# Performance work log

Measured on AMD Instinct MI355X. Metric: run time of the kernel, lower is better.

The kernel has to match this reference:

```python
import jax, jax.numpy as jnp
import numpy as np

N = 32768      # nodes
DIN = 256      # in_channels (space dim; hyperbolic input has DIN+1 dims)
DOUT = 256     # out_channels
H = 8          # num_heads
K = 1.0        # Lorentz curvature manifold.k
P = 2          # power_k
EPS = 1e-6


def _lorentz(key, n, d):
    # random point on Lorentz manifold: time = sqrt(||space||^2 + k)
    s = jax.random.normal(key, (n, d), jnp.float32)
    t = jnp.sqrt(jnp.sum(s * s, -1, keepdims=True) + K)
    return jnp.concatenate([t, s], -1)


def setup_inputs() -> dict:
    key = jax.random.key(0)
    ks = jax.random.split(key, 8)
    sc = 0.02
    return {
        "query_input": _lorentz(ks[0], N, DIN),
        "source_input": _lorentz(ks[1], N, DIN),
        "Wq_w": jax.random.normal(ks[2], (H, DOUT, DIN + 1), jnp.float32) * sc,
        "Wq_b": jnp.zeros((H, DOUT), jnp.float32),
        "Wk_w": jax.random.normal(ks[3], (H, DOUT, DIN + 1), jnp.float32) * sc,
        "Wk_b": jnp.zeros((H, DOUT), jnp.float32),
        "Wv_w": jax.random.normal(ks[4], (H, DOUT, DIN + 1), jnp.float32) * sc,
        "Wv_b": jnp.zeros((H, DOUT), jnp.float32),
        "norm_scale": jnp.ones((), jnp.float32),
        "v_map_w": jax.random.normal(ks[5], (DOUT, DIN), jnp.float32) * sc,
        "v_map_b": jnp.zeros((DOUT,), jnp.float32),
        "final_w": jax.random.normal(ks[6], (DOUT, H * DOUT), jnp.float32) * sc,
        "final_b": jnp.zeros((DOUT,), jnp.float32),
    }


def _hyp_linear(x, W, b):
    # HypLinear for all heads at once. x: [N, Din+1], W: [H, Dout, Din+1], b: [H, Dout]
    xs = jnp.einsum('ni,hoi->nho', x, W) + b              # space part [N,H,Dout]
    xt = jnp.sqrt(jnp.sum(xs * xs, -1, keepdims=True) + K)  # Lorentz time
    return jnp.concatenate([xt, xs], -1)                  # [N,H,Dout+1]


def _fp(x, p=P):
    # fp(x) = ||x|| / ||x^p|| * x^p  (per-vector rescaled power map)
    norm_x = jnp.linalg.norm(x, axis=-1, keepdims=True)
    xp = x ** p
    norm_xp = jnp.linalg.norm(xp, axis=-1, keepdims=True)
    return norm_x / norm_xp * xp


def reference(query_input, source_input, Wq_w, Wq_b, Wk_w, Wk_b, Wv_w, Wv_b,
              norm_scale, v_map_w, v_map_b, final_w, final_b):
    q = _hyp_linear(query_input, Wq_w, Wq_b)    # [N,H,D+1]
    k = _hyp_linear(source_input, Wk_w, Wk_b)   # [N,H,D+1]
    v = _hyp_linear(source_input, Wv_w, Wv_b)   # [N,H,D+1]

    # linear_focus_attention: drop time dim
    qs, ks_, vs = q[..., 1:], k[..., 1:], v[..., 1:]     # [N,H,D]
    dscale = jnp.abs(norm_scale) + EPS
    phi_q = _fp((jax.nn.relu(qs) + EPS) / dscale)
    phi_k = _fp((jax.nn.relu(ks_) + EPS) / dscale)

    ktv = jnp.einsum('nhm,nhd->hmd', phi_k, vs)          # [H,D,D]
    numerator = jnp.einsum('nhm,hmd->nhd', phi_q, ktv)   # [N,H,D]
    denominator = jnp.einsum('nhd,hd->nh', phi_q, jnp.sum(phi_k, 0))[..., None]
    attn = numerator / (denominator + EPS)

    vss = vs @ v_map_w.T + v_map_b                       # v_map_mlp(v)
    attn = attn + vss

    # trans_heads_concat -> final_linear
    out = attn.reshape(N, H * DOUT) @ final_w.T + final_b  # [N,Dout]

    # lift back to Lorentz manifold
    t = jnp.sqrt(jnp.sum(out * out, -1, keepdims=True) + K)
    return jnp.concatenate([t, out], -1)                 # [N,Dout+1]
```

## Files before the change

kernel.cpp:

```cpp
#include <hip/hip_runtime.h>
#include <hip/hip_bf16.h>


#define EPSF 1e-6f

typedef __attribute__((ext_vector_type(8))) short bf16x8;
typedef __attribute__((ext_vector_type(8))) unsigned short u16x8;
typedef __attribute__((ext_vector_type(4))) float f32x4;
typedef float f32x4a __attribute__((ext_vector_type(4), aligned(4)));

__device__ __forceinline__ float b2f(unsigned short u) {
    union { unsigned int i; float f; } c;
    c.i = ((unsigned int)u) << 16;
    return c.f;
}
__device__ __forceinline__ unsigned short f2b(float f) {
    __hip_bfloat16 h = __float2bfloat16(f);
    union { __hip_bfloat16 h; unsigned short u; } c;
    c.h = h;
    return c.u;
}

__global__ void zero_kernel(float* __restrict__ p, int n) {
    int i = blockIdx.x * 256 + threadIdx.x;
    if (i < n) p[i] = 0.f;
}

__global__ __launch_bounds__(256) void wconv_kernel(
    const float* __restrict__ Wq, const float* __restrict__ Wk, const float* __restrict__ Wv,
    const float* __restrict__ Bq, const float* __restrict__ Bk, const float* __restrict__ Bv,
    unsigned short* __restrict__ Wbf, float* __restrict__ biasAll)
{
    const int t = threadIdx.x;
    const int b = blockIdx.x;
    if (b < 6144) {
        const int mat = b >> 11, lr = b & 2047;
        const float* Ws = (mat == 0 ? Wq : mat == 1 ? Wk : Wv) + (size_t)lr * 257;
        Wbf[(size_t)b * 288 + t] = f2b(Ws[t]);
        if (t < 32) {
            float v = (t == 0) ? Ws[256] : 0.f;
            Wbf[(size_t)b * 288 + 256 + t] = f2b(v);
        }
    } else {
        const int e = (b - 6144) * 256 + t;
        const int mat = e >> 11, r = e & 2047;
        biasAll[e] = (mat == 0 ? Bq : mat == 1 ? Bk : Bv)[r];
    }
}

__global__ __launch_bounds__(256) void proj_mfma(
    const float* __restrict__ X,
    const unsigned short* __restrict__ Wbase,
    const float* __restrict__ biasBase,
    unsigned short* __restrict__ outA,
    unsigned short* __restrict__ outB,
    int splitCol)
{
    __shared__ __align__(16) unsigned short lA[128 * 40];
    __shared__ __align__(16) unsigned short lB[128 * 40];
    const int t = threadIdx.x;
    const int m0 = blockIdx.x * 128;
    const int c0 = blockIdx.y * 128;
    const int lane = t & 63, w = t >> 6;
    const int wm = (w >> 1) * 64, wn = (w & 1) * 64;
    const int l15 = lane & 15, q = lane >> 4;

    f32x4 acc[4][4] = {};

    for (int ks = 0; ks < 9; ++ks) {
        const int k0 = ks * 32;
        if (ks < 8) {
#pragma unroll
            for (int qq = 0; qq < 2; ++qq) {
                const int e = t + qq * 256;
                const int row = e >> 2, kg = (e & 3) * 8;
                f32x4a x0 = *(const f32x4a*)(X + (size_t)(m0 + row) * 257 + k0 + kg);
                f32x4a x1 = *(const f32x4a*)(X + (size_t)(m0 + row) * 257 + k0 + kg + 4);
                u16x8 pk;
                pk[0] = f2b(x0[0]); pk[1] = f2b(x0[1]);
                pk[2] = f2b(x0[2]); pk[3] = f2b(x0[3]);
                pk[4] = f2b(x1[0]); pk[5] = f2b(x1[1]);
                pk[6] = f2b(x1[2]); pk[7] = f2b(x1[3]);
                *(u16x8*)(&lA[row * 40 + kg]) = pk;
            }
        } else {
#pragma unroll
            for (int qq = 0; qq < 2; ++qq) {
                const int e = t + qq * 256;
                const int row = e >> 2, part = e & 3;
                u16x8 z = {};
                if (part == 0) z[0] = f2b(X[(size_t)(m0 + row) * 257 + 256]);
                *(u16x8*)(&lA[row * 40 + part * 8]) = z;
            }
        }
#pragma unroll
        for (int qq = 0; qq < 2; ++qq) {
            const int e = t + qq * 256;
            const int row = e >> 2, kg = (e & 3) * 8;
            *(u16x8*)(&lB[row * 40 + kg]) =
                *(const u16x8*)(Wbase + (size_t)(c0 + row) * 288 + k0 + kg);
        }
        __syncthreads();
        bf16x8 af[4], bfr[4];
#pragma unroll
        for (int i = 0; i < 4; ++i)
            af[i] = *(const bf16x8*)(&lA[(wm + i * 16 + l15) * 40 + q * 8]);
#pragma unroll
        for (int j = 0; j < 4; ++j)
            bfr[j] = *(const bf16x8*)(&lB[(wn + j * 16 + l15) * 40 + q * 8]);
#pragma unroll
        for (int i = 0; i < 4; ++i)
#pragma unroll
            for (int j = 0; j < 4; ++j)
                acc[i][j] = __builtin_amdgcn_mfma_f32_16x16x32_bf16(af[i], bfr[j], acc[i][j], 0, 0, 0);
        __syncthreads();
    }

#pragma unroll
    for (int j = 0; j < 4; ++j) {
        const int cg = c0 + wn + j * 16 + l15;
        const float bias = biasBase[cg];
        unsigned short* dst;
        int cd;
        if (cg < splitCol) { dst = outA; cd = cg; }
        else               { dst = outB; cd = cg - 2048; }
#pragma unroll
        for (int i = 0; i < 4; ++i)
#pragma unroll
            for (int r = 0; r < 4; ++r) {
                const int n = m0 + wm + i * 16 + q * 4 + r;
                dst[(size_t)n * 2048 + cd] = f2b(acc[i][j][r] + bias);
            }
    }
}

__global__ __launch_bounds__(256) void proj_phi(
    const float* __restrict__ X,
    const unsigned short* __restrict__ Wbase,
    const float* __restrict__ biasBase,
    unsigned short* __restrict__ outbuf,
    const float* __restrict__ nsc,
    const float* __restrict__ colsum_in,
    float* __restrict__ colsum_rep,
    int mode)
{
    __shared__ __align__(16) unsigned short lA[64 * 40];
    __shared__ __align__(16) unsigned short lB[256 * 40];
    __shared__ float reds2[4][64];
    __shared__ float reds4[4][64];
    __shared__ float rowv[64];

    const int t = threadIdx.x;
    const int m0 = blockIdx.x * 64;
    const int h  = blockIdx.y;
    const int lane = t & 63, w = t >> 6;
    const int wn = w * 64;
    const int l15 = lane & 15, q = lane >> 4;

    f32x4 acc[4][4] = {};

    for (int ks = 0; ks < 9; ++ks) {
        const int k0 = ks * 32;
        if (ks < 8) {
            const int row = t >> 2, kg = (t & 3) * 8;
            f32x4a x0 = *(const f32x4a*)(X + (size_t)(m0 + row) * 257 + k0 + kg);
            f32x4a x1 = *(const f32x4a*)(X + (size_t)(m0 + row) * 257 + k0 + kg + 4);
            u16x8 pk;
            pk[0] = f2b(x0[0]); pk[1] = f2b(x0[1]);
            pk[2] = f2b(x0[2]); pk[3] = f2b(x0[3]);
            pk[4] = f2b(x1[0]); pk[5] = f2b(x1[1]);
            pk[6] = f2b(x1[2]); pk[7] = f2b(x1[3]);
            *(u16x8*)(&lA[row * 40 + kg]) = pk;
        } else {
            const int row = t >> 2, part = t & 3;
            u16x8 z = {};
            if (part == 0) z[0] = f2b(X[(size_t)(m0 + row) * 257 + 256]);
            *(u16x8*)(&lA[row * 40 + part * 8]) = z;
        }
#pragma unroll
        for (int qq = 0; qq < 4; ++qq) {
            const int e = t + qq * 256;
            const int row = e >> 2, kg = (e & 3) * 8;
            *(u16x8*)(&lB[row * 40 + kg]) =
                *(const u16x8*)(Wbase + (size_t)(h * 256 + row) * 288 + k0 + kg);
        }
        __syncthreads();
        bf16x8 af[4], bfr[4];
#pragma unroll
        for (int i = 0; i < 4; ++i)
            af[i] = *(const bf16x8*)(&lA[(i * 16 + l15) * 40 + q * 8]);
#pragma unroll
        for (int j = 0; j < 4; ++j)
            bfr[j] = *(const bf16x8*)(&lB[(wn + j * 16 + l15) * 40 + q * 8]);
#pragma unroll
        for (int i = 0; i < 4; ++i)
#pragma unroll
            for (int j = 0; j < 4; ++j)
                acc[i][j] = __builtin_amdgcn_mfma_f32_16x16x32_bf16(af[i], bfr[j], acc[i][j], 0, 0, 0);
        __syncthreads();
    }

    const float c = fabsf(nsc[0]) + EPSF;
    float bias[4];
#pragma unroll
    for (int j = 0; j < 4; ++j) bias[j] = biasBase[h * 256 + wn + j * 16 + l15];

    float a2[4][4], a4[4][4];
#pragma unroll
    for (int i = 0; i < 4; ++i)
#pragma unroll
        for (int r = 0; r < 4; ++r) { a2[i][r] = 0.f; a4[i][r] = 0.f; }
#pragma unroll
    for (int i = 0; i < 4; ++i)
#pragma unroll
        for (int j = 0; j < 4; ++j)
#pragma unroll
            for (int r = 0; r < 4; ++r) {
                float uu = fmaxf(acc[i][j][r] + bias[j], 0.f) + EPSF;
                float p2 = uu * uu;
                acc[i][j][r] = p2;
                a2[i][r] += p2;
                a4[i][r] += p2 * p2;
            }
#pragma unroll
    for (int m = 1; m <= 8; m <<= 1) {
#pragma unroll
        for (int i = 0; i < 4; ++i)
#pragma unroll
            for (int r = 0; r < 4; ++r) {
                a2[i][r] += __shfl_xor(a2[i][r], m, 64);
                a4[i][r] += __shfl_xor(a4[i][r], m, 64);
            }
    }
    if (l15 == 0) {
#pragma unroll
        for (int i = 0; i < 4; ++i)
#pragma unroll
            for (int r = 0; r < 4; ++r) {
                reds2[w][i * 16 + q * 4 + r] = a2[i][r];
                reds4[w][i * 16 + q * 4 + r] = a4[i][r];
            }
    }
    __syncthreads();
    if (t < 64) {
        float s2t = reds2[0][t] + reds2[1][t] + reds2[2][t] + reds2[3][t];
        float s4t = reds4[0][t] + reds4[1][t] + reds4[2][t] + reds4[3][t];
        rowv[t] = sqrtf(s2t) / (c * sqrtf(s4t));
    }
    __syncthreads();
    float sc_[4][4];
#pragma unroll
    for (int i = 0; i < 4; ++i)
#pragma unroll
        for (int r = 0; r < 4; ++r) sc_[i][r] = rowv[i * 16 + q * 4 + r];

    if (mode == 0) {
        float colp[4];
#pragma unroll
        for (int j = 0; j < 4; ++j) colp[j] = 0.f;
#pragma unroll
        for (int i = 0; i < 4; ++i)
#pragma unroll
            for (int j = 0; j < 4; ++j)
#pragma unroll
                for (int r = 0; r < 4; ++r) {
                    float ph = acc[i][j][r] * sc_[i][r];
                    acc[i][j][r] = ph;
                    colp[j] += ph;
                }
#pragma unroll
        for (int i = 0; i < 4; ++i)
#pragma unroll
            for (int j = 0; j < 4; ++j)
#pragma unroll
                for (int r = 0; r < 4; ++r) {
                    const int n = m0 + i * 16 + q * 4 + r;
                    outbuf[(size_t)n * 2048 + h * 256 + wn + j * 16 + l15] = f2b(acc[i][j][r]);
                }
#pragma unroll
        for (int j = 0; j < 4; ++j) {
            colp[j] += __shfl_xor(colp[j], 16, 64);
            colp[j] += __shfl_xor(colp[j], 32, 64);
        }
        if (q == 0) {
            float* dst = colsum_rep + (size_t)(blockIdx.x & 7) * 2048;
#pragma unroll
            for (int j = 0; j < 4; ++j)
                atomicAdd(&dst[h * 256 + wn + j * 16 + l15], colp[j]);
        }
    } else {
        float cs[4];
#pragma unroll
        for (int j = 0; j < 4; ++j) cs[j] = colsum_in[h * 256 + wn + j * 16 + l15];
        float dp[4][4];
#pragma unroll
        for (int i = 0; i < 4; ++i)
#pragma unroll
            for (int r = 0; r < 4; ++r) dp[i][r] = 0.f;
#pragma unroll
        for (int i = 0; i < 4; ++i)
#pragma unroll
            for (int j = 0; j < 4; ++j)
#pragma unroll
                for (int r = 0; r < 4; ++r) {
                    float ph = acc[i][j][r] * sc_[i][r];
                    acc[i][j][r] = ph;
                    dp[i][r] += ph * cs[j];
                }
#pragma unroll
        for (int m = 1; m <= 8; m <<= 1) {
#pragma unroll
            for (int i = 0; i < 4; ++i)
#pragma unroll
                for (int r = 0; r < 4; ++r)
                    dp[i][r] += __shfl_xor(dp[i][r], m, 64);
        }
        if (l15 == 0) {
#pragma unroll
            for (int i = 0; i < 4; ++i)
#pragma unroll
                for (int r = 0; r < 4; ++r)
                    reds2[w][i * 16 + q * 4 + r] = dp[i][r];
        }
        __syncthreads();
        if (t < 64) {
            float dt = reds2[0][t] + reds2[1][t] + reds2[2][t] + reds2[3][t];
            rowv[t] = 1.f / (dt + EPSF);
        }
        __syncthreads();
#pragma unroll
        for (int i = 0; i < 4; ++i)
#pragma unroll
            for (int r = 0; r < 4; ++r) sc_[i][r] = rowv[i * 16 + q * 4 + r];
#pragma unroll
        for (int i = 0; i < 4; ++i)
#pragma unroll
            for (int j = 0; j < 4; ++j)
#pragma unroll
                for (int r = 0; r < 4; ++r) {
                    const int n = m0 + i * 16 + q * 4 + r;
                    outbuf[(size_t)n * 2048 + h * 256 + wn + j * 16 + l15] =
                        f2b(acc[i][j][r] * sc_[i][r]);
                }
    }
}

__global__ __launch_bounds__(256) void merge_colsum(
    const float* __restrict__ rep, float* __restrict__ out)
{
    const int cidx = blockIdx.x * 256 + threadIdx.x;
    float s = 0.f;
#pragma unroll
    for (int r = 0; r < 8; ++r) s += rep[(size_t)r * 2048 + cidx];
    out[cidx] = s;
}

__device__ __forceinline__ void ktv_load(
    const unsigned short* __restrict__ pA, const unsigned short* __restrict__ pB,
    int n0, int oct0,
    u16x8& A0, u16x8& A1, u16x8& B0, u16x8& B1)
{
    const unsigned short* a0 = pA + (size_t)(n0 + oct0 * 8) * 2048;
    const unsigned short* b0 = pB + (size_t)(n0 + oct0 * 8) * 2048;
    const unsigned short* a1 = a0 + (size_t)16 * 2048;
    const unsigned short* b1 = b0 + (size_t)16 * 2048;
#pragma unroll
    for (int j = 0; j < 8; ++j) {
        A0[j] = a0[(size_t)j * 2048];
        B0[j] = b0[(size_t)j * 2048];
        A1[j] = a1[(size_t)j * 2048];
        B1[j] = b1[(size_t)j * 2048];
    }
}

__global__ __launch_bounds__(256) void ktv_mfma(
    const unsigned short* __restrict__ phiK,
    const unsigned short* __restrict__ vsb,
    float* __restrict__ ktv)
{
    __shared__ __align__(16) unsigned short lAT[128 * 40];
    __shared__ __align__(16) unsigned short lBT[128 * 40];
    const int t = threadIdx.x;
    const int h = blockIdx.y;
    const int split = blockIdx.x >> 2;
    const int tile = blockIdx.x & 3;
    const int m0 = (tile >> 1) * 128, d0 = (tile & 1) * 128;
    const int chh = h * 256;
    const int lane = t & 63, w = t >> 6;
    const int wm = (w >> 1) * 64, wn = (w & 1) * 64;
    const int l15 = lane & 15, q8 = (lane >> 4) * 8;

    const int col = t & 127;
    const int oct0 = t >> 7;
    const unsigned short* pA = phiK + chh + m0 + col;
    const unsigned short* pB = vsb  + chh + d0 + col;

    f32x4 acc[4][4] = {};
    const int nbeg = split * 512;

    u16x8 cA0, cA1, cB0, cB1, nA0, nA1, nB0, nB1;
    ktv_load(pA, pB, nbeg, oct0, cA0, cA1, cB0, cB1);

    for (int it = 0; it < 16; ++it) {
        *(u16x8*)(&lAT[col * 40 + oct0 * 8])       = cA0;
        *(u16x8*)(&lBT[col * 40 + oct0 * 8])       = cB0;
        *(u16x8*)(&lAT[col * 40 + (oct0 + 2) * 8]) = cA1;
        *(u16x8*)(&lBT[col * 40 + (oct0 + 2) * 8]) = cB1;
        if (it < 15)
            ktv_load(pA, pB, nbeg + (it + 1) * 32, oct0, nA0, nA1, nB0, nB1);
        __syncthreads();
        bf16x8 af[4], bfr[4];
#pragma unroll
        for (int i = 0; i < 4; ++i)
            af[i] = *(const bf16x8*)(&lAT[(wm + i * 16 + l15) * 40 + q8]);
#pragma unroll
        for (int j = 0; j < 4; ++j)
            bfr[j] = *(const bf16x8*)(&lBT[(wn + j * 16 + l15) * 40 + q8]);
#pragma unroll
        for (int i = 0; i < 4; ++i)
#pragma unroll
            for (int j = 0; j < 4; ++j)
                acc[i][j] = __builtin_amdgcn_mfma_f32_16x16x32_bf16(af[i], bfr[j], acc[i][j], 0, 0, 0);
        __syncthreads();
        if (it < 15) { cA0 = nA0; cA1 = nA1; cB0 = nB0; cB1 = nB1; }
    }
#pragma unroll
    for (int i = 0; i < 4; ++i)
#pragma unroll
        for (int j = 0; j < 4; ++j)
#pragma unroll
            for (int r = 0; r < 4; ++r) {
                const int m = m0 + wm + i * 16 + (lane >> 4) * 4 + r;
                const int d = d0 + wn + j * 16 + l15;
                atomicAdd(&ktv[((size_t)chh + m) * 256 + d], acc[i][j][r]);
            }
}

__device__ __forceinline__ void fin_load(
    const unsigned short* __restrict__ Abuf, const unsigned short* __restrict__ W2T,
    int n0, int d0, int t, int k0,
    u16x8& A0, u16x8& A1, u16x8& B)
{
    {
        const int row = t >> 2, kg = (t & 3) * 8;
        A0 = *(const u16x8*)(Abuf + (size_t)(n0 + row) * 2048 + ((k0 + kg) & 2047));
    }
    {
        const int e = t + 256;
        const int row = e >> 2, kg = (e & 3) * 8;
        A1 = *(const u16x8*)(Abuf + (size_t)(n0 + row) * 2048 + ((k0 + kg) & 2047));
    }
    {
        const int row = t >> 2, kg = (t & 3) * 8;
        B = *(const u16x8*)(W2T + (size_t)(d0 + row) * 4096 + k0 + kg);
    }
}

__global__ __launch_bounds__(256) void final_mfma(
    const unsigned short* __restrict__ Abuf,
    const unsigned short* __restrict__ W2T,
    int kbeg, int kend, int accumulate,
    float* __restrict__ outp)
{
    __shared__ __align__(16) unsigned short lA[128 * 40];
    __shared__ __align__(16) unsigned short lB[64 * 40];
    const int t = threadIdx.x;
    const int n0 = blockIdx.x * 128;
    const int d0 = blockIdx.y * 64;
    const int lane = t & 63, w = t >> 6;
    const int wm = w * 32;
    const int l15 = lane & 15, q = lane >> 4;

    f32x4 acc[2][4] = {};
    u16x8 cA0, cA1, cB, nA0, nA1, nB;
    fin_load(Abuf, W2T, n0, d0, t, kbeg, cA0, cA1, cB);

    for (int k0 = kbeg; k0 < kend; k0 += 32) {
        {
            const int row = t >> 2, kg = (t & 3) * 8;
            *(u16x8*)(&lA[row * 40 + kg]) = cA0;
            *(u16x8*)(&lB[row * 40 + kg]) = cB;
        }
        {
            const int e = t + 256;
            const int row = e >> 2, kg = (e & 3) * 8;
            *(u16x8*)(&lA[row * 40 + kg]) = cA1;
        }
        if (k0 + 32 < kend)
            fin_load(Abuf, W2T, n0, d0, t, k0 + 32, nA0, nA1, nB);
        __syncthreads();
        bf16x8 af[2], bfr[4];
#pragma unroll
        for (int i = 0; i < 2; ++i)
            af[i] = *(const bf16x8*)(&lA[(wm + i * 16 + l15) * 40 + q * 8]);
#pragma unroll
        for (int j = 0; j < 4; ++j)
            bfr[j] = *(const bf16x8*)(&lB[(j * 16 + l15) * 40 + q * 8]);
#pragma unroll
        for (int i = 0; i < 2; ++i)
#pragma unroll
            for (int j = 0; j < 4; ++j)
                acc[i][j] = __builtin_amdgcn_mfma_f32_16x16x32_bf16(af[i], bfr[j], acc[i][j], 0, 0, 0);
        __syncthreads();
        if (k0 + 32 < kend) { cA0 = nA0; cA1 = nA1; cB = nB; }
    }
#pragma unroll
    for (int i = 0; i < 2; ++i)
#pragma unroll
        for (int j = 0; j < 4; ++j)
#pragma unroll
            for (int r = 0; r < 4; ++r) {
                const int n = n0 + wm + i * 16 + q * 4 + r;
                const int d = d0 + j * 16 + l15;
                float* p = &outp[(size_t)n * 257 + 1 + d];
                if (accumulate) *p += acc[i][j][r];
                else            *p  = acc[i][j][r];
            }
}

__global__ __launch_bounds__(256) void w2g_kernel(
    const float* __restrict__ vmw,
    const float* __restrict__ fw,
    unsigned short* __restrict__ W2T)
{
    const int t = threadIdx.x;
    const int h = blockIdx.x >> 3;
    const int i0 = (blockIdx.x & 7) * 32;

    __shared__ __align__(16) float xlds[16][40];
    __shared__ float wlds[256][17];

    float acc[32];
#pragma unroll
    for (int r = 0; r < 32; ++r) acc[r] = 0.f;

    const int ar = t >> 3;
    const int ak = (t & 7) * 2;
    const int wk = t & 15;
    const int wo = (t >> 4) * 16;

    for (int d0 = 0; d0 < 256; d0 += 16) {
        xlds[ak][ar]     = vmw[(size_t)(d0 + ak) * 256 + i0 + ar];
        xlds[ak + 1][ar] = vmw[(size_t)(d0 + ak + 1) * 256 + i0 + ar];
#pragma unroll
        for (int j = 0; j < 16; ++j)
            wlds[wo + j][wk] = fw[(size_t)(wo + j) * 2048 + h * 256 + d0 + wk];
        __syncthreads();
#pragma unroll
        for (int kk = 0; kk < 16; ++kk) {
            float bv = wlds[t][kk];
            const float4* xr = (const float4*)(&xlds[kk][0]);
#pragma unroll
            for (int g = 0; g < 8; ++g) {
                float4 xv = xr[g];
                acc[g * 4 + 0] = fmaf(xv.x, bv, acc[g * 4 + 0]);
                acc[g * 4 + 1] = fmaf(xv.y, bv, acc[g * 4 + 1]);
                acc[g * 4 + 2] = fmaf(xv.z, bv, acc[g * 4 + 2]);
                acc[g * 4 + 3] = fmaf(xv.w, bv, acc[g * 4 + 3]);
            }
        }
        __syncthreads();
    }
#pragma unroll
    for (int r = 0; r < 32; ++r)
        W2T[(size_t)t * 4096 + 2048 + h * 256 + i0 + r] = f2b(acc[r]);
}

__global__ __launch_bounds__(256) void bias2_kernel(
    const float* __restrict__ vmb, const float* __restrict__ fw,
    const float* __restrict__ fb, float* __restrict__ bias2)
{
    const int o = blockIdx.x;
    const int t = threadIdx.x;
    float s = 0.f;
#pragma unroll
    for (int i = 0; i < 8; ++i)
        s += fw[(size_t)o * 2048 + t + i * 256];
    s *= vmb[t];
#pragma unroll
    for (int off = 32; off > 0; off >>= 1) s += __shfl_down(s, off, 64);
    __shared__ float r4[4];
    if ((t & 63) == 0) r4[t >> 6] = s;
    __syncthreads();
    if (t == 0) bias2[o] = fb[o] + r4[0] + r4[1] + r4[2] + r4[3];
}

__global__ __launch_bounds__(256) void w2u_kernel(
    const float* __restrict__ ktv,
    const float* __restrict__ fw,
    unsigned short* __restrict__ W2T)
{
    const int t = threadIdx.x;
    const int h = blockIdx.x >> 3;
    const int m0 = (blockIdx.x & 7) * 32;

    __shared__ __align__(16) float xlds[16][40];
    __shared__ float wlds[256][17];

    float acc[32];
#pragma unroll
    for (int r = 0; r < 32; ++r) acc[r] = 0.f;

    const int ar = t >> 3;
    const int ak = (t & 7) * 2;
    const int wk = t & 15;
    const int wo = (t >> 4) * 16;

    for (int d0 = 0; d0 < 256; d0 += 16) {
        {
            const float* src = ktv + (size_t)(h * 256 + m0 + ar) * 256 + d0 + ak;
            xlds[ak][ar]     = src[0];
            xlds[ak + 1][ar] = src[1];
        }
#pragma unroll
        for (int j = 0; j < 16; ++j)
            wlds[wo + j][wk] = fw[(size_t)(wo + j) * 2048 + h * 256 + d0 + wk];
        __syncthreads();
#pragma unroll
        for (int kk = 0; kk < 16; ++kk) {
            float bv = wlds[t][kk];
            const float4* xr = (const float4*)(&xlds[kk][0]);
#pragma unroll
            for (int g = 0; g < 8; ++g) {
                float4 xv = xr[g];
                acc[g * 4 + 0] = fmaf(xv.x, bv, acc[g * 4 + 0]);
                acc[g * 4 + 1] = fmaf(xv.y, bv, acc[g * 4 + 1]);
                acc[g * 4 + 2] = fmaf(xv.z, bv, acc[g * 4 + 2]);
                acc[g * 4 + 3] = fmaf(xv.w, bv, acc[g * 4 + 3]);
            }
        }
        __syncthreads();
    }
#pragma unroll
    for (int r = 0; r < 32; ++r)
        W2T[(size_t)t * 4096 + h * 256 + m0 + r] = f2b(acc[r]);
}

__global__ __launch_bounds__(256) void lift_kernel(
    const float* __restrict__ bias2, float* __restrict__ outp)
{
    const int t = threadIdx.x;
    const int lane = t & 63;
    const int w = t >> 6;
    const int n0 = blockIdx.x * 64 + w * 16;
    float b[4];
#pragma unroll
    for (int j = 0; j < 4; ++j) b[j] = bias2[lane + j * 64];
    for (int r = 0; r < 16; ++r) {
        float* row = outp + (size_t)(n0 + r) * 257;
        float v[4];
        float s = 0.f;
#pragma unroll
        for (int j = 0; j < 4; ++j) {
            v[j] = row[1 + lane + j * 64] + b[j];
            s = fmaf(v[j], v[j], s);
        }
#pragma unroll
        for (int off = 32; off > 0; off >>= 1) s += __shfl_down(s, off, 64);
#pragma unroll
        for (int j = 0; j < 4; ++j) row[1 + lane + j * 64] = v[j];
        if (lane == 0) row[0] = sqrtf(s + 1.0f);
    }
}

extern "C" void kernel_launch(void* const* d_in, const int* in_sizes, int n_in,
                              void* d_out, int out_size, void* d_ws, size_t ws_size,
                              hipStream_t stream)
{
    const float* xq  = (const float*)d_in[0];
    const float* xs  = (const float*)d_in[1];
    const float* Wq  = (const float*)d_in[2];
    const float* Bq  = (const float*)d_in[3];
    const float* Wk  = (const float*)d_in[4];
    const float* Bk  = (const float*)d_in[5];
    const float* Wv  = (const float*)d_in[6];
    const float* Bv  = (const float*)d_in[7];
    const float* nsc = (const float*)d_in[8];
    const float* vmw = (const float*)d_in[9];
    const float* vmb = (const float*)d_in[10];
    const float* fw  = (const float*)d_in[11];
    const float* fb  = (const float*)d_in[12];
    float* outp = (float*)d_out;

    char* ws = (char*)d_ws;
    float* ktv          = (float*)(ws + 0);
    float* colrep       = (float*)(ws + 2097152);
    float* colsum       = (float*)(ws + 2162688);
    float* bias2        = (float*)(ws + 2170880);
    float* biasAll      = (float*)(ws + 2171904);
    unsigned short* W2T = (unsigned short*)(ws + 2196480);
    unsigned short* Wbf = (unsigned short*)(ws + 4293632);
    const size_t fixedBytes = 7832576;

    int CH = 2048;
    if (ws_size >= fixedBytes + (size_t)8192 * 8192) CH = 8192;
    else if (ws_size >= fixedBytes + (size_t)4096 * 8192) CH = 4096;
    const int NCHK = 32768 / CH;
    unsigned short* phibuf = (unsigned short*)(ws + fixedBytes);
    unsigned short* vsbuf  = (unsigned short*)(ws + fixedBytes + (size_t)CH * 4096);

    zero_kernel<<<dim3(2112), 256, 0, stream>>>(ktv, 540672);
    wconv_kernel<<<dim3(6168), 256, 0, stream>>>(Wq, Wk, Wv, Bq, Bk, Bv, Wbf, biasAll);
    w2g_kernel<<<dim3(64), 256, 0, stream>>>(vmw, fw, W2T);
    bias2_kernel<<<dim3(256), 256, 0, stream>>>(vmb, fw, fb, bias2);

    for (int c = 0; c < NCHK; ++c) {
        const float* xs_c = xs + (size_t)c * CH * 257;
        float* out_c = outp + (size_t)c * CH * 257;
        proj_phi<<<dim3(CH / 64, 8), 256, 0, stream>>>(
            xs_c, Wbf + (size_t)2048 * 288, biasAll + 2048, phibuf,
            nsc, nullptr, colrep, 0);
        proj_mfma<<<dim3(CH / 128, 16), 256, 0, stream>>>(
            xs_c, Wbf + (size_t)4096 * 288, biasAll + 4096, vsbuf, vsbuf, 4096);
        ktv_mfma<<<dim3((CH / 512) * 4, 8), 256, 0, stream>>>(phibuf, vsbuf, ktv);
        final_mfma<<<dim3(CH / 128, 4), 256, 0, stream>>>(vsbuf, W2T, 2048, 4096, 0, out_c);
    }

    merge_colsum<<<dim3(8), 256, 0, stream>>>(colrep, colsum);
    w2u_kernel<<<dim3(64), 256, 0, stream>>>(ktv, fw, W2T);

    for (int c = 0; c < NCHK; ++c) {
        const float* xq_c = xq + (size_t)c * CH * 257;
        float* out_c = outp + (size_t)c * CH * 257;
        proj_phi<<<dim3(CH / 64, 8), 256, 0, stream>>>(
            xq_c, Wbf, biasAll, phibuf,
            nsc, colsum, nullptr, 1);
        final_mfma<<<dim3(CH / 128, 4), 256, 0, stream>>>(phibuf, W2T, 0, 2048, 1, out_c);
    }

    lift_kernel<<<dim3(512), 256, 0, stream>>>(bias2, outp);
}
```

Baseline: 1.004 ms.

## Write phi_k and V transposed so ktv loads contiguous vectors

```diff
diff --git a/kernel.cpp b/kernel.cpp
--- a/kernel.cpp
+++ b/kernel.cpp
@@ -52,12 +52,13 @@
     const float* __restrict__ X,
     const unsigned short* __restrict__ Wbase,
     const float* __restrict__ biasBase,
-    unsigned short* __restrict__ outA,
-    unsigned short* __restrict__ outB,
-    int splitCol)
-{
-    __shared__ __align__(16) unsigned short lA[128 * 40];
-    __shared__ __align__(16) unsigned short lB[128 * 40];
+    unsigned short* __restrict__ out,
+    unsigned short* __restrict__ outT,
+    int CH)
+{
+    __shared__ __align__(16) unsigned short smem[10240];
+    unsigned short* lA = smem;
+    unsigned short* lB = smem + 128 * 40;
     const int t = threadIdx.x;
     const int m0 = blockIdx.x * 128;
     const int c0 = blockIdx.y * 128;
@@ -120,17 +121,43 @@
     for (int j = 0; j < 4; ++j) {
         const int cg = c0 + wn + j * 16 + l15;
         const float bias = biasBase[cg];
-        unsigned short* dst;
-        int cd;
-        if (cg < splitCol) { dst = outA; cd = cg; }
-        else               { dst = outB; cd = cg - 2048; }
 #pragma unroll
         for (int i = 0; i < 4; ++i)
 #pragma unroll
             for (int r = 0; r < 4; ++r) {
+                acc[i][j][r] += bias;
                 const int n = m0 + wm + i * 16 + q * 4 + r;
-                dst[(size_t)n * 2048 + cd] = f2b(acc[i][j][r] + bias);
-            }
+                out[(size_t)n * 2048 + cg] = f2b(acc[i][j][r]);
+            }
+    }
+
+#pragma unroll
+    for (int p = 0; p < 2; ++p) {
+        __syncthreads();
+        if ((w >> 1) == p) {
+#pragma unroll
+            for (int i = 0; i < 4; ++i)
+#pragma unroll
+                for (int j = 0; j < 4; ++j) {
+                    const int cl = wn + j * 16 + l15;
+#pragma unroll
+                    for (int r2 = 0; r2 < 4; r2 += 2) {
+                        const int nl = i * 16 + q * 4 + r2;
+                        const unsigned int pk =
+                            (unsigned int)f2b(acc[i][j][r2]) |
+                            ((unsigned int)f2b(acc[i][j][r2 + 1]) << 16);
+                        *(unsigned int*)(&smem[cl * 64 + (((nl >> 3) ^ (cl & 7)) << 3) + (nl & 7)]) = pk;
+                    }
+                }
+        }
+        __syncthreads();
+#pragma unroll
+        for (int k = 0; k < 4; ++k) {
+            const int task = k * 256 + t;
+            const int cl = task >> 3, nq = task & 7;
+            *(u16x8*)(outT + (size_t)(c0 + cl) * CH + m0 + p * 64 + nq * 8) =
+                *(const u16x8*)(&smem[cl * 64 + ((nq ^ (cl & 7)) << 3)]);
+        }
     }
 }
 
@@ -142,13 +169,14 @@
     const float* __restrict__ nsc,
     const float* __restrict__ colsum_in,
     float* __restrict__ colsum_rep,
-    int mode)
-{
-    __shared__ __align__(16) unsigned short lA[64 * 40];
-    __shared__ __align__(16) unsigned short lB[256 * 40];
+    int mode, int CH)
+{
+    __shared__ __align__(16) unsigned short smem[16384];
     __shared__ float reds2[4][64];
     __shared__ float reds4[4][64];
     __shared__ float rowv[64];
+    unsigned short* lA = smem;
+    unsigned short* lB = smem + 64 * 40;
 
     const int t = threadIdx.x;
     const int m0 = blockIdx.x * 64;
@@ -217,10 +245,10 @@
 #pragma unroll
             for (int r = 0; r < 4; ++r) {
                 float uu = fmaxf(acc[i][j][r] + bias[j], 0.f) + EPSF;
-                float p2 = uu * uu;
-                acc[i][j][r] = p2;
-                a2[i][r] += p2;
-                a4[i][r] += p2 * p2;
+                float q2 = uu * uu;
+                acc[i][j][r] = q2;
+                a2[i][r] += q2;
+                a4[i][r] += q2 * q2;
             }
 #pragma unroll
     for (int m = 1; m <= 8; m <<= 1) {
@@ -271,12 +299,25 @@
 #pragma unroll
         for (int i = 0; i < 4; ++i)
 #pragma unroll
-            for (int j = 0; j < 4; ++j)
-#pragma unroll
-                for (int r = 0; r < 4; ++r) {
-                    const int n = m0 + i * 16 + q * 4 + r;
-                    outbuf[(size_t)n * 2048 + h * 256 + wn + j * 16 + l15] = f2b(acc[i][j][r]);
+            for (int j = 0; j < 4; ++j) {
+                const int cl = wn + j * 16 + l15;
+#pragma unroll
+                for (int r2 = 0; r2 < 4; r2 += 2) {
+                    const int nl = i * 16 + q * 4 + r2;
+                    const unsigned int pk =
+                        (unsigned int)f2b(acc[i][j][r2]) |
+                        ((unsigned int)f2b(acc[i][j][r2 + 1]) << 16);
+                    *(unsigned int*)(&smem[cl * 64 + (((nl >> 3) ^ (cl & 7)) << 3) + (nl & 7)]) = pk;
                 }
+            }
+        __syncthreads();
+#pragma unroll
+        for (int k = 0; k < 8; ++k) {
+            const int task = k * 256 + t;
+            const int cl = task >> 3, nq = task & 7;
+            *(u16x8*)(outbuf + (size_t)(h * 256 + cl) * CH + m0 + nq * 8) =
+                *(const u16x8*)(&smem[cl * 64 + ((nq ^ (cl & 7)) << 3)]);
+        }
 #pragma unroll
         for (int j = 0; j < 4; ++j) {
             colp[j] += __shfl_xor(colp[j], 16, 64);
@@ -355,31 +396,13 @@
     out[cidx] = s;
 }
 
-__device__ __forceinline__ void ktv_load(
-    const unsigned short* __restrict__ pA, const unsigned short* __restrict__ pB,
-    int n0, int oct0,
-    u16x8& A0, u16x8& A1, u16x8& B0, u16x8& B1)
-{
-    const unsigned short* a0 = pA + (size_t)(n0 + oct0 * 8) * 2048;
-    const unsigned short* b0 = pB + (size_t)(n0 + oct0 * 8) * 2048;
-    const unsigned short* a1 = a0 + (size_t)16 * 2048;
-    const unsigned short* b1 = b0 + (size_t)16 * 2048;
-#pragma unroll
-    for (int j = 0; j < 8; ++j) {
-        A0[j] = a0[(size_t)j * 2048];
-        B0[j] = b0[(size_t)j * 2048];
-        A1[j] = a1[(size_t)j * 2048];
-        B1[j] = b1[(size_t)j * 2048];
-    }
-}
-
 __global__ __launch_bounds__(256) void ktv_mfma(
-    const unsigned short* __restrict__ phiK,
-    const unsigned short* __restrict__ vsb,
-    float* __restrict__ ktv)
-{
-    __shared__ __align__(16) unsigned short lAT[128 * 40];
-    __shared__ __align__(16) unsigned short lBT[128 * 40];
+    const unsigned short* __restrict__ phiT,
+    const unsigned short* __restrict__ vsT,
+    float* __restrict__ ktv, int CH)
+{
+    __shared__ __align__(16) unsigned short lAT[128 * 64];
+    __shared__ __align__(16) unsigned short lBT[128 * 64];
     const int t = threadIdx.x;
     const int h = blockIdx.y;
     const int split = blockIdx.x >> 2;
@@ -388,49 +411,56 @@
     const int chh = h * 256;
     const int lane = t & 63, w = t >> 6;
     const int wm = (w >> 1) * 64, wn = (w & 1) * 64;
-    const int l15 = lane & 15, q8 = (lane >> 4) * 8;
-
-    const int col = t & 127;
-    const int oct0 = t >> 7;
-    const unsigned short* pA = phiK + chh + m0 + col;
-    const unsigned short* pB = vsb  + chh + d0 + col;
+    const int l15 = lane & 15, q = lane >> 4;
+    const int sl7 = l15 & 7;
+
+    const int scg  = t >> 3;
+    const int snq  = t & 7;
+    const int sbase = scg * 64 + ((snq ^ (scg & 7)) << 3);
 
     f32x4 acc[4][4] = {};
-    const int nbeg = split * 512;
-
-    u16x8 cA0, cA1, cB0, cB1, nA0, nA1, nB0, nB1;
-    ktv_load(pA, pB, nbeg, oct0, cA0, cA1, cB0, cB1);
-
-    for (int it = 0; it < 16; ++it) {
-        *(u16x8*)(&lAT[col * 40 + oct0 * 8])       = cA0;
-        *(u16x8*)(&lBT[col * 40 + oct0 * 8])       = cB0;
-        *(u16x8*)(&lAT[col * 40 + (oct0 + 2) * 8]) = cA1;
-        *(u16x8*)(&lBT[col * 40 + (oct0 + 2) * 8]) = cB1;
-        if (it < 15)
-            ktv_load(pA, pB, nbeg + (it + 1) * 32, oct0, nA0, nA1, nB0, nB1);
-        __syncthreads();
-        bf16x8 af[4], bfr[4];
-#pragma unroll
-        for (int i = 0; i < 4; ++i)
-            af[i] = *(const bf16x8*)(&lAT[(wm + i * 16 + l15) * 40 + q8]);
+    const int nb0 = split * 256;
+
+    for (int it = 0; it < 4; ++it) {
+        const int nb = nb0 + it * 64;
+        u16x8 ra[4], rb[4];
+#pragma unroll
+        for (int k = 0; k < 4; ++k) {
+            const size_t col = (size_t)(k * 32 + scg);
+            ra[k] = *(const u16x8*)(phiT + (chh + m0 + col) * CH + nb + snq * 8);
+            rb[k] = *(const u16x8*)(vsT  + (chh + d0 + col) * CH + nb + snq * 8);
+        }
+#pragma unroll
+        for (int k = 0; k < 4; ++k) {
+            *(u16x8*)(&lAT[k * 2048 + sbase]) = ra[k];
+            *(u16x8*)(&lBT[k * 2048 + sbase]) = rb[k];
+        }
+        __syncthreads();
+#pragma unroll
+        for (int sub = 0; sub < 2; ++sub) {
+            const int slot = ((sub * 4 + q) ^ sl7) << 3;
+            bf16x8 af[4], bfr[4];
+#pragma unroll
+            for (int i = 0; i < 4; ++i)
+                af[i] = *(const bf16x8*)(&lAT[(wm + i * 16 + l15) * 64 + slot]);
+#pragma unroll
+            for (int j = 0; j < 4; ++j)
+                bfr[j] = *(const bf16x8*)(&lBT[(wn + j * 16 + l15) * 64 + slot]);
+#pragma unroll
+            for (int i = 0; i < 4; ++i)
+#pragma unroll
+                for (int j = 0; j < 4; ++j)
+                    acc[i][j] = __builtin_amdgcn_mfma_f32_16x16x32_bf16(af[i], bfr[j], acc[i][j], 0, 0, 0);
+        }
+        __syncthreads();
+    }
+#pragma unroll
+    for (int i = 0; i < 4; ++i)
 #pragma unroll
         for (int j = 0; j < 4; ++j)
-            bfr[j] = *(const bf16x8*)(&lBT[(wn + j * 16 + l15) * 40 + q8]);
-#pragma unroll
-        for (int i = 0; i < 4; ++i)
-#pragma unroll
-            for (int j = 0; j < 4; ++j)
-                acc[i][j] = __builtin_amdgcn_mfma_f32_16x16x32_bf16(af[i], bfr[j], acc[i][j], 0, 0, 0);
-        __syncthreads();
-        if (it < 15) { cA0 = nA0; cA1 = nA1; cB0 = nB0; cB1 = nB1; }
-    }
-#pragma unroll
-    for (int i = 0; i < 4; ++i)
-#pragma unroll
-        for (int j = 0; j < 4; ++j)
 #pragma unroll
             for (int r = 0; r < 4; ++r) {
-                const int m = m0 + wm + i * 16 + (lane >> 4) * 4 + r;
+                const int m = m0 + wm + i * 16 + q * 4 + r;
                 const int d = d0 + wn + j * 16 + l15;
                 atomicAdd(&ktv[((size_t)chh + m) * 256 + d], acc[i][j][r]);
             }
@@ -693,11 +723,12 @@
     const size_t fixedBytes = 7832576;
 
     int CH = 2048;
-    if (ws_size >= fixedBytes + (size_t)8192 * 8192) CH = 8192;
-    else if (ws_size >= fixedBytes + (size_t)4096 * 8192) CH = 4096;
+    if (ws_size >= fixedBytes + (size_t)8192 * 12288) CH = 8192;
+    else if (ws_size >= fixedBytes + (size_t)4096 * 12288) CH = 4096;
     const int NCHK = 32768 / CH;
     unsigned short* phibuf = (unsigned short*)(ws + fixedBytes);
     unsigned short* vsbuf  = (unsigned short*)(ws + fixedBytes + (size_t)CH * 4096);
+    unsigned short* vsT    = (unsigned short*)(ws + fixedBytes + (size_t)CH * 8192);
 
     zero_kernel<<<dim3(2112), 256, 0, stream>>>(ktv, 540672);
     wconv_kernel<<<dim3(6168), 256, 0, stream>>>(Wq, Wk, Wv, Bq, Bk, Bv, Wbf, biasAll);
@@ -709,10 +740,10 @@
         float* out_c = outp + (size_t)c * CH * 257;
         proj_phi<<<dim3(CH / 64, 8), 256, 0, stream>>>(
             xs_c, Wbf + (size_t)2048 * 288, biasAll + 2048, phibuf,
-            nsc, nullptr, colrep, 0);
+            nsc, nullptr, colrep, 0, CH);
         proj_mfma<<<dim3(CH / 128, 16), 256, 0, stream>>>(
-            xs_c, Wbf + (size_t)4096 * 288, biasAll + 4096, vsbuf, vsbuf, 4096);
-        ktv_mfma<<<dim3((CH / 512) * 4, 8), 256, 0, stream>>>(phibuf, vsbuf, ktv);
+            xs_c, Wbf + (size_t)4096 * 288, biasAll + 4096, vsbuf, vsT, CH);
+        ktv_mfma<<<dim3((CH / 256) * 4, 8), 256, 0, stream>>>(phibuf, vsT, ktv, CH);
         final_mfma<<<dim3(CH / 128, 4), 256, 0, stream>>>(vsbuf, W2T, 2048, 4096, 0, out_c);
     }
 
@@ -724,7 +755,7 @@
         float* out_c = outp + (size_t)c * CH * 257;
         proj_phi<<<dim3(CH / 64, 8), 256, 0, stream>>>(
             xq_c, Wbf, biasAll, phibuf,
-            nsc, colsum, nullptr, 1);
+            nsc, colsum, nullptr, 1, CH);
         final_mfma<<<dim3(CH / 128, 4), 256, 0, stream>>>(phibuf, W2T, 0, 2048, 1, out_c);
     }
 
```

Measured after the change: 1.296 ms. +29.1%, slower.
